# Kernel optimization log

Measured on AMD Instinct MI355X. Metric: run time of the kernel, lower is better.

Reference implementation:

```python
import jax, jax.numpy as jnp
import numpy as np


def setup_inputs() -> dict:
    key = jax.random.key(0)
    k1, k2 = jax.random.split(key)
    N, M, D = 8192, 8192, 128
    z_anc = jax.random.normal(k1, (N, D), dtype=jnp.float32)
    z_pos_neg = jax.random.normal(k2, (M, D), dtype=jnp.float32)
    return {"z_anc": z_anc, "z_pos_neg": z_pos_neg}


def reference(z_anc, z_pos_neg):
    # -||a_i - b_j||_2 computed via the GEMM expansion
    # ||a-b||^2 = ||a||^2 + ||b||^2 - 2 a.b  (avoids the O(N*M*D) broadcast)
    a2 = jnp.sum(z_anc * z_anc, axis=-1)          # [N]
    b2 = jnp.sum(z_pos_neg * z_pos_neg, axis=-1)  # [M]
    ab = jnp.einsum("nd,md->nm", z_anc, z_pos_neg)  # [N, M]
    d2 = jnp.maximum(a2[:, None] + b2[None, :] - 2.0 * ab, 0.0)
    return -jnp.sqrt(d2)
```

## Files before the change

kernel.cpp:

```cpp
#include <hip/hip_runtime.h>
#include <hip/hip_bf16.h>

#define D_DIM 128
#define TILE 128
#define LT_PAD 4

typedef __attribute__((ext_vector_type(8))) short short8;
typedef __attribute__((ext_vector_type(4))) float floatx4;

__global__ void prep_kernel(const float* __restrict__ za, const float* __restrict__ zb,
                            __hip_bfloat16* __restrict__ abf, __hip_bfloat16* __restrict__ bbf,
                            float* __restrict__ a2, float* __restrict__ b2, int N) {
    int r = blockIdx.x * 4 + (threadIdx.x >> 6);
    int lane = threadIdx.x & 63;
    const float* src; __hip_bfloat16* dst; float* nrm; int row;
    if (r < N) { src = za; dst = abf; nrm = a2; row = r; }
    else       { src = zb; dst = bbf; nrm = b2; row = r - N; }
    const float2 v = ((const float2*)(src + (size_t)row * D_DIM))[lane];
    __hip_bfloat16 h0 = __float2bfloat16(v.x);
    __hip_bfloat16 h1 = __float2bfloat16(v.y);
    float f0 = __bfloat162float(h0), f1 = __bfloat162float(h1);
    float ss = f0 * f0 + f1 * f1;
    ushort2 st;
    st.x = *(const unsigned short*)&h0;
    st.y = *(const unsigned short*)&h1;
    ((ushort2*)(dst + (size_t)row * D_DIM))[lane] = st;
    #pragma unroll
    for (int off = 32; off; off >>= 1) ss += __shfl_down(ss, off, 64);
    if (lane == 0) nrm[row] = ss;
}

__global__ __launch_bounds__(256, 3)
void dist_kernel(const __hip_bfloat16* __restrict__ abf, const __hip_bfloat16* __restrict__ bbf,
                 const float* __restrict__ a2, const float* __restrict__ b2,
                 float* __restrict__ out, int M) {
    __shared__ float lt[64][128 + LT_PAD];

    const int rowBase = blockIdx.y * TILE;
    const int colBase = blockIdx.x * TILE;
    const int tid  = threadIdx.x;
    const int wave = tid >> 6;
    const int lane = tid & 63;
    const int wn = (wave >> 1) * 64;
    const int wm = (wave & 1) * 64;
    const int lrow = lane & 15;
    const int lk8  = (lane >> 4) * 8;
    const int mq   = (lane >> 4) * 4;

    int aOff[4], bOff[4];
    #pragma unroll
    for (int j = 0; j < 4; ++j) {
        aOff[j] = (rowBase + wn + j * 16 + lrow) * D_DIM;
        bOff[j] = (colBase + wm + j * 16 + lrow) * D_DIM;
    }

    floatx4 acc[4][4] = {};
    #pragma unroll
    for (int ks = 0; ks < 4; ++ks) {
        const int k0 = ks * 32 + lk8;
        short8 afr[4], bfr[4];
        #pragma unroll
        for (int jm = 0; jm < 4; ++jm)
            afr[jm] = *(const short8*)(bbf + (bOff[jm] + k0));
        #pragma unroll
        for (int jn = 0; jn < 4; ++jn)
            bfr[jn] = *(const short8*)(abf + (aOff[jn] + k0));
        #pragma unroll
        for (int jm = 0; jm < 4; ++jm)
            #pragma unroll
            for (int jn = 0; jn < 4; ++jn)
                acc[jm][jn] = __builtin_amdgcn_mfma_f32_16x16x32_bf16(afr[jm], bfr[jn], acc[jm][jn], 0, 0, 0);
    }

    float an[4];
    floatx4 bq[4];
    #pragma unroll
    for (int jn = 0; jn < 4; ++jn) an[jn] = a2[rowBase + wn + jn * 16 + lrow];
    #pragma unroll
    for (int jm = 0; jm < 4; ++jm) bq[jm] = *(const floatx4*)(b2 + colBase + wm + jm * 16 + mq);

    const int myChunk = wave >> 1;
    #pragma unroll
    for (int c = 0; c < 2; ++c) {
        if (myChunk == c) {
            #pragma unroll
            for (int jn = 0; jn < 4; ++jn) {
                const int nl = jn * 16 + lrow;
                #pragma unroll
                for (int jm = 0; jm < 4; ++jm) {
                    floatx4 v;
                    #pragma unroll
                    for (int r = 0; r < 4; ++r) {
                        float d2 = an[jn] + bq[jm][r] - 2.0f * acc[jm][jn][r];
                        d2 = fmaxf(d2, 0.0f);
                        v[r] = -__builtin_amdgcn_sqrtf(d2);
                    }
                    *(floatx4*)(&lt[nl][wm + jm * 16 + mq]) = v;
                }
            }
        }
        __syncthreads();
        const size_t base = (size_t)(rowBase + c * 64) * (size_t)M + (size_t)colBase;
        #pragma unroll
        for (int p = 0; p < 8; ++p) {
            const int row = p * 8 + (tid >> 5);
            const int col = (tid & 31) * 4;
            const floatx4 v = *(const floatx4*)(&lt[row][col]);
            __builtin_nontemporal_store(v, (floatx4*)(out + base + (size_t)row * M + col));
        }
        if (c == 0) __syncthreads();
    }
}

extern "C" void kernel_launch(void* const* d_in, const int* in_sizes, int n_in,
                              void* d_out, int out_size, void* d_ws, size_t ws_size,
                              hipStream_t stream) {
    const float* za = (const float*)d_in[0];
    const float* zb = (const float*)d_in[1];
    const int N = in_sizes[0] / D_DIM;
    const int M = in_sizes[1] / D_DIM;
    float* out = (float*)d_out;

    char* ws = (char*)d_ws;
    __hip_bfloat16* abf = (__hip_bfloat16*)ws;
    __hip_bfloat16* bbf = (__hip_bfloat16*)(ws + (size_t)N * D_DIM * sizeof(__hip_bfloat16));
    float* a2 = (float*)(ws + (size_t)(N + M) * D_DIM * sizeof(__hip_bfloat16));
    float* b2 = a2 + N;

    prep_kernel<<<(N + M) / 4, 256, 0, stream>>>(za, zb, abf, bbf, a2, b2, N);

    dim3 grid(M / TILE, N / TILE);
    dist_kernel<<<grid, 256, 0, stream>>>(abf, bbf, a2, b2, out, M);
}
```

Baseline: 330.7 us.

## Stage A/B bf16 tiles in LDS and write full output tile in one pass

Cooperatively loads the 128x128 bf16 A and B tiles into padded shared memory once, and MFMA fragments are then read from LDS instead of directly from global memory. The same LDS buffer is reused for a full 128-row output staging tile, so all waves compute at once and a single store phase replaces the two-chunk alternation. Output stores switch from nontemporal to regular stores, and occupancy hint drops from 3 to 2 blocks because of the larger LDS footprint (~68KB).

```diff
diff --git a/kernel.cpp b/kernel.cpp
--- a/kernel.cpp
+++ b/kernel.cpp
@@ -3,7 +3,8 @@
 
 #define D_DIM 128
 #define TILE 128
-#define LT_PAD 4
+#define LDS_K (D_DIM + 8)
+#define LT_K  (D_DIM + 4)
 
 typedef __attribute__((ext_vector_type(8))) short short8;
 typedef __attribute__((ext_vector_type(4))) float floatx4;
@@ -30,15 +31,33 @@
     if (lane == 0) nrm[row] = ss;
 }
 
-__global__ __launch_bounds__(256, 3)
+__global__ __launch_bounds__(256, 2)
 void dist_kernel(const __hip_bfloat16* __restrict__ abf, const __hip_bfloat16* __restrict__ bbf,
                  const float* __restrict__ a2, const float* __restrict__ b2,
                  float* __restrict__ out, int M) {
-    __shared__ float lt[64][128 + LT_PAD];
+    __shared__ __align__(16) char smem[2 * TILE * LDS_K * sizeof(__hip_bfloat16)];
+    typedef __hip_bfloat16 bfrow_t[LDS_K];
+    typedef float frow_t[LT_K];
+    bfrow_t* As = reinterpret_cast<bfrow_t*>(smem);
+    bfrow_t* Bs = reinterpret_cast<bfrow_t*>(smem + TILE * LDS_K * sizeof(__hip_bfloat16));
+    frow_t*  lt = reinterpret_cast<frow_t*>(smem);
 
     const int rowBase = blockIdx.y * TILE;
     const int colBase = blockIdx.x * TILE;
-    const int tid  = threadIdx.x;
+    const int tid = threadIdx.x;
+
+    #pragma unroll
+    for (int pass = 0; pass < 8; ++pass) {
+        int idx = pass * 256 + tid;
+        int row = idx >> 4;
+        int kc  = (idx & 15) * 8;
+        uint4 va = *(const uint4*)(abf + ((size_t)(rowBase + row) * D_DIM + kc));
+        *(uint4*)(&As[row][kc]) = va;
+        uint4 vb = *(const uint4*)(bbf + ((size_t)(colBase + row) * D_DIM + kc));
+        *(uint4*)(&Bs[row][kc]) = vb;
+    }
+    __syncthreads();
+
     const int wave = tid >> 6;
     const int lane = tid & 63;
     const int wn = (wave >> 1) * 64;
@@ -47,13 +66,6 @@
     const int lk8  = (lane >> 4) * 8;
     const int mq   = (lane >> 4) * 4;
 
-    int aOff[4], bOff[4];
-    #pragma unroll
-    for (int j = 0; j < 4; ++j) {
-        aOff[j] = (rowBase + wn + j * 16 + lrow) * D_DIM;
-        bOff[j] = (colBase + wm + j * 16 + lrow) * D_DIM;
-    }
-
     floatx4 acc[4][4] = {};
     #pragma unroll
     for (int ks = 0; ks < 4; ++ks) {
@@ -61,10 +73,10 @@
         short8 afr[4], bfr[4];
         #pragma unroll
         for (int jm = 0; jm < 4; ++jm)
-            afr[jm] = *(const short8*)(bbf + (bOff[jm] + k0));
+            afr[jm] = *(const short8*)(&Bs[wm + jm * 16 + lrow][k0]);
         #pragma unroll
         for (int jn = 0; jn < 4; ++jn)
-            bfr[jn] = *(const short8*)(abf + (aOff[jn] + k0));
+            bfr[jn] = *(const short8*)(&As[wn + jn * 16 + lrow][k0]);
         #pragma unroll
         for (int jm = 0; jm < 4; ++jm)
             #pragma unroll
@@ -79,36 +91,32 @@
     #pragma unroll
     for (int jm = 0; jm < 4; ++jm) bq[jm] = *(const floatx4*)(b2 + colBase + wm + jm * 16 + mq);
 
-    const int myChunk = wave >> 1;
+    __syncthreads();
+
     #pragma unroll
-    for (int c = 0; c < 2; ++c) {
-        if (myChunk == c) {
+    for (int jn = 0; jn < 4; ++jn) {
+        const int nl = wn + jn * 16 + lrow;
+        #pragma unroll
+        for (int jm = 0; jm < 4; ++jm) {
+            floatx4 v;
             #pragma unroll
-            for (int jn = 0; jn < 4; ++jn) {
-                const int nl = jn * 16 + lrow;
-                #pragma unroll
-                for (int jm = 0; jm < 4; ++jm) {
-                    floatx4 v;
-                    #pragma unroll
-                    for (int r = 0; r < 4; ++r) {
-                        float d2 = an[jn] + bq[jm][r] - 2.0f * acc[jm][jn][r];
-                        d2 = fmaxf(d2, 0.0f);
-                        v[r] = -__builtin_amdgcn_sqrtf(d2);
-                    }
-                    *(floatx4*)(&lt[nl][wm + jm * 16 + mq]) = v;
-                }
+            for (int r = 0; r < 4; ++r) {
+                float d2 = an[jn] + bq[jm][r] - 2.0f * acc[jm][jn][r];
+                d2 = fmaxf(d2, 0.0f);
+                v[r] = -__builtin_amdgcn_sqrtf(d2);
             }
+            *(floatx4*)(&lt[nl][wm + jm * 16 + mq]) = v;
         }
-        __syncthreads();
-        const size_t base = (size_t)(rowBase + c * 64) * (size_t)M + (size_t)colBase;
-        #pragma unroll
-        for (int p = 0; p < 8; ++p) {
-            const int row = p * 8 + (tid >> 5);
-            const int col = (tid & 31) * 4;
-            const floatx4 v = *(const floatx4*)(&lt[row][col]);
-            __builtin_nontemporal_store(v, (floatx4*)(out + base + (size_t)row * M + col));
-        }
-        if (c == 0) __syncthreads();
+    }
+    __syncthreads();
+
+    const size_t base = (size_t)rowBase * (size_t)M + (size_t)colBase;
+    #pragma unroll
+    for (int p = 0; p < 16; ++p) {
+        const int row = p * 8 + (tid >> 5);
+        const int col = (tid & 31) * 4;
+        const floatx4 v = *(const floatx4*)(&lt[row][col]);
+        *(floatx4*)(out + base + (size_t)row * M + col) = v;
     }
 }
 
```

Measured after the change: 284.7 us. -13.9%, faster.
